# Performance work log

Hardware: AMD Instinct MI355X
Metric: run time of the kernel (lower is better)

## Reference

```python
import jax, jax.numpy as jnp
import numpy as np

E, T, D, H = 32, 65536, 512, 1024


def setup_inputs() -> dict:
    key = jax.random.key(0)
    k = jax.random.split(key, 7)
    norm = lambda kk, shp, sc: (jax.random.normal(kk, shp, jnp.float32) * sc)
    x = norm(k[0], (T, D), 1.0)
    w1 = norm(k[1], (E, D, H), D ** -0.5)   # per-expert up-proj (gate branch)
    b1 = norm(k[2], (E, H), 0.02)
    w3 = norm(k[3], (E, D, H), D ** -0.5)   # per-expert up-proj (linear branch)
    b3 = norm(k[4], (E, H), 0.02)
    w2 = norm(k[5], (E, H, D), H ** -0.5)   # per-expert down-proj
    b2 = norm(k[6], (E, D), 0.02)
    # tokens are pre-sorted by expert; uniform dispatch of T//E tokens per expert
    group_sizes = jnp.full((E,), T // E, jnp.int32)
    return dict(x=x, w1=w1, b1=b1, w3=w3, b3=b3, w2=w2, b2=b2,
                group_sizes=group_sizes)


def reference(x, w1, b1, w3, b3, w2, b2, group_sizes):
    # expert id per token, derived from contiguous group sizes
    bounds = jnp.cumsum(group_sizes)                       # [E]
    seg = jnp.searchsorted(bounds, jnp.arange(x.shape[0]), side='right')  # [T]
    # grouped GEMMs: per-expert weight bank applied to its contiguous token slab
    h1 = jax.lax.ragged_dot(x, w1, group_sizes) + b1[seg]  # [T,H]
    h3 = jax.lax.ragged_dot(x, w3, group_sizes) + b3[seg]  # [T,H]
    h = jax.nn.silu(h1) * h3                               # SwiGLU gate
    out = jax.lax.ragged_dot(h, w2, group_sizes) + b2[seg] # [T,D]
    return out
```

## Files before the change

kernel.cpp:

```cpp
#include <hip/hip_runtime.h>
#include <hip/hip_bf16.h>

#define TOK 65536
#define NE  32
#define DD  512
#define HH  1024
#define TPE 2048

typedef short s16x8  __attribute__((ext_vector_type(8)));
typedef float f32x16 __attribute__((ext_vector_type(16)));
using u16 = unsigned short;
using u32 = unsigned int;

__device__ __forceinline__ u16 f2bf(float f) {
  __bf16 h = (__bf16)f;
  return __builtin_bit_cast(u16, h);
}
__device__ __forceinline__ u32 pk2(float lo, float hi) {
  return (u32)f2bf(lo) | ((u32)f2bf(hi) << 16);
}
__device__ __forceinline__ int swz(int row, int colb) {
  return (row << 7) + (colb ^ ((row & 7) << 4));
}

#define MFMA(a, b, c) __builtin_amdgcn_mfma_f32_32x32x16_bf16(a, b, c, 0, 0, 0)
#define GLD(src, dst) __builtin_amdgcn_global_load_lds( \
    (const __attribute__((address_space(1))) void*)(src), \
    (__attribute__((address_space(3))) void*)(dst), 16, 0, 0)


__global__ __launch_bounds__(256) void p1_cvt_x(
    const float* __restrict__ x, u16* __restrict__ xb) {
  const size_t i = ((size_t)blockIdx.x * 256 + threadIdx.x) * 8;
  const float4 a = *(const float4*)(x + i);
  const float4 b = *(const float4*)(x + i + 4);
  uint4 v;
  v.x = pk2(a.x, a.y); v.y = pk2(a.z, a.w);
  v.z = pk2(b.x, b.y); v.w = pk2(b.z, b.w);
  *(uint4*)(xb + i) = v;
}

__global__ __launch_bounds__(256) void p2_w13t(
    const float* __restrict__ w1, const float* __restrict__ w3,
    u16* __restrict__ w13t) {
  __shared__ __align__(16) u16 L1[64 * 72], L3[64 * 72];
  const int bid = blockIdx.x;
  const int e = bid >> 7, rr = bid & 127;
  const int d0 = (rr & 7) << 6, h0 = (rr >> 3) << 6;
  const int t = threadIdx.x;
  const float* const s1 = w1 + (size_t)e * DD * HH + (size_t)d0 * HH + h0;
  const float* const s3 = w3 + (size_t)e * DD * HH + (size_t)d0 * HH + h0;
  const int cg = (t & 15) << 2, rbase = t >> 4;
#pragma unroll
  for (int j = 0; j < 4; ++j) {
    const int dr = rbase + (j << 4);
    const float4 a = *(const float4*)(s1 + (size_t)dr * HH + cg);
    const float4 b = *(const float4*)(s3 + (size_t)dr * HH + cg);
    L1[(cg + 0) * 72 + dr] = f2bf(a.x); L1[(cg + 1) * 72 + dr] = f2bf(a.y);
    L1[(cg + 2) * 72 + dr] = f2bf(a.z); L1[(cg + 3) * 72 + dr] = f2bf(a.w);
    L3[(cg + 0) * 72 + dr] = f2bf(b.x); L3[(cg + 1) * 72 + dr] = f2bf(b.y);
    L3[(cg + 2) * 72 + dr] = f2bf(b.z); L3[(cg + 3) * 72 + dr] = f2bf(b.w);
  }
  __syncthreads();
  u16* const dst = w13t + (size_t)e * (2 * HH) * DD;
  const int cb8 = (t & 7) << 3;
#pragma unroll
  for (int j = 0; j < 2; ++j) {
    const int nloc = (t >> 3) + (j << 5);
    const int n = h0 + nloc;
    const int R1 = ((n >> 5) << 6) + (n & 31);
    const uint4 v1 = *(const uint4*)(L1 + nloc * 72 + cb8);
    const uint4 v3 = *(const uint4*)(L3 + nloc * 72 + cb8);
    *(uint4*)(dst + (size_t)R1 * DD + d0 + cb8) = v1;
    *(uint4*)(dst + (size_t)(R1 + 32) * DD + d0 + cb8) = v3;
  }
}

__global__ __launch_bounds__(256) void p3_w2t(
    const float* __restrict__ w2, u16* __restrict__ w2t) {
  __shared__ __align__(16) u16 L[64 * 72];
  const int bid = blockIdx.x;
  const int e = bid >> 7, rr = bid & 127;
  const int d0 = (rr & 7) << 6, h0 = (rr >> 3) << 6;
  const int t = threadIdx.x;
  const float* const s = w2 + (size_t)e * HH * DD + (size_t)h0 * DD + d0;
  const int cg = (t & 15) << 2, rbase = t >> 4;
#pragma unroll
  for (int j = 0; j < 4; ++j) {
    const int hr = rbase + (j << 4);
    const float4 a = *(const float4*)(s + (size_t)hr * DD + cg);
    L[(cg + 0) * 72 + hr] = f2bf(a.x); L[(cg + 1) * 72 + hr] = f2bf(a.y);
    L[(cg + 2) * 72 + hr] = f2bf(a.z); L[(cg + 3) * 72 + hr] = f2bf(a.w);
  }
  __syncthreads();
  u16* const dst = w2t + (size_t)e * DD * HH;
  const int cb8 = (t & 7) << 3;
#pragma unroll
  for (int j = 0; j < 2; ++j) {
    const int dloc = (t >> 3) + (j << 5);
    const uint4 v = *(const uint4*)(L + dloc * 72 + cb8);
    *(uint4*)(dst + (size_t)(d0 + dloc) * HH + h0 + cb8) = v;
  }
}

template <int MODE>
__global__ __launch_bounds__(256, 3) void gemm_tile(
    const u16* __restrict__ A, const u16* __restrict__ Bm,
    const float* __restrict__ bx, const float* __restrict__ by,
    void* __restrict__ outp) {
  constexpr int K = MODE ? HH : DD;
  constexpr int NT = K >> 6;
  constexpr int NBLK = MODE ? 4 : 16;
  __shared__ __align__(16) char lds[32768];
  char* const As = lds;
  char* const Bs = lds + 16384;

  const int bid = blockIdx.x;
  const int e   = bid / (16 * NBLK);
  const int rr  = bid % (16 * NBLK);
  const int m_t = rr & 15;
  const int n_t = rr >> 4;
  const int rowbase = e * TPE + (m_t << 7);

  const int t = threadIdx.x, wv = t >> 6, lane = t & 63;
  const int l31 = lane & 31, half = lane >> 5;
  const int wm = wv >> 1, wn = wv & 1;

  const u16* const Abase = A + (size_t)rowbase * K;
  const u16* const Bbase = Bm + (size_t)e * NBLK * 128 * K + (size_t)n_t * 128 * K;

  int soff[4], lb[4];
#pragma unroll
  for (int j = 0; j < 4; ++j) {
    const int idx = (j << 8) + t;
    const int r = idx >> 3;
    const int cb = ((idx & 7) << 4) ^ ((r & 7) << 4);
    soff[j] = r * K + (cb >> 1);
    lb[j] = ((j << 8) + (wv << 6)) << 4;
  }

  f32x16 c00 = {}, c01 = {}, c10 = {}, c11 = {};
  const int sw  = (l31 & 7) << 4;
  const int ra0 = ((wm << 6) + l31) << 7, ra1 = ra0 + (32 << 7);
  const int rb0 = ((wn << 6) + l31) << 7, rb1 = rb0 + (32 << 7);

  for (int kt = 0; kt < NT; ++kt) {
    const u16* const Ak = Abase + (kt << 6);
    const u16* const Bk = Bbase + (kt << 6);
#pragma unroll
    for (int j = 0; j < 4; ++j) {
      GLD(Ak + soff[j], As + lb[j]);
      GLD(Bk + soff[j], Bs + lb[j]);
    }
    __syncthreads();
#pragma unroll
    for (int ks = 0; ks < 4; ++ks) {
      const int ko = ((ks << 5) + (half << 4)) ^ sw;
      const s16x8 a0 = *(const s16x8*)(As + ra0 + ko);
      const s16x8 a1 = *(const s16x8*)(As + ra1 + ko);
      const s16x8 b0 = *(const s16x8*)(Bs + rb0 + ko);
      const s16x8 b1 = *(const s16x8*)(Bs + rb1 + ko);
      c00 = MFMA(a0, b0, c00); c01 = MFMA(a0, b1, c01);
      c10 = MFMA(a1, b0, c10); c11 = MFMA(a1, b1, c11);
    }
    __syncthreads();
  }

  if constexpr (MODE == 0) {
    const int gcol = (n_t << 6) + (wn << 5) + l31;
    const float bv1 = bx[e * HH + gcol];
    const float bv3 = by[e * HH + gcol];
    u16* const hp = (u16*)outp;
#pragma unroll
    for (int mf = 0; mf < 2; ++mf) {
      const f32x16 A1 = mf ? c10 : c00;
      const f32x16 A3 = mf ? c11 : c01;
#pragma unroll
      for (int rg = 0; rg < 16; ++rg) {
        const int grow = rowbase + (wm << 6) + (mf << 5) +
                         (rg & 3) + ((rg >> 2) << 3) + (half << 2);
        const float s1 = A1[rg] + bv1;
        const float s3 = A3[rg] + bv3;
        hp[(size_t)grow * HH + gcol] = f2bf(s1 * s3 / (1.0f + __expf(-s1)));
      }
    }
  } else {
    float* const op = (float*)outp;
#pragma unroll
    for (int mf = 0; mf < 2; ++mf) {
#pragma unroll
      for (int fn = 0; fn < 2; ++fn) {
        const f32x16 C = mf ? (fn ? c11 : c10) : (fn ? c01 : c00);
        const int gcol = (n_t << 7) + (wn << 6) + (fn << 5) + l31;
        const float bv = bx[e * DD + gcol];
#pragma unroll
        for (int rg = 0; rg < 16; ++rg) {
          const int grow = rowbase + (wm << 6) + (mf << 5) +
                           (rg & 3) + ((rg >> 2) << 3) + (half << 2);
          op[(size_t)grow * DD + gcol] = C[rg] + bv;
        }
      }
    }
  }
}

__global__ __launch_bounds__(256, 2) void k1_up_swiglu(
    const float* __restrict__ x,  const float* __restrict__ w1,
    const float* __restrict__ b1, const float* __restrict__ w3,
    const float* __restrict__ b3, u16* __restrict__ hbuf) {
  __shared__ __align__(16) char lds[32768];
  char* const As  = lds;
  char* const B1s = lds + 16384;
  char* const B3s = lds + 24576;
  const int bid = blockIdx.x;
  const int e = bid >> 8, rr = bid & 255;
  const int m_t = rr & 15, n_t = rr >> 4;
  const int rowbase = e * TPE + (m_t << 7), colbase = n_t << 6;
  const int t = threadIdx.x, wv = t >> 6, lane = t & 63;
  const int l31 = lane & 31, half = lane >> 5;
  const int wm = wv >> 1, wn = wv & 1;
  const int ag = t & 15, am0 = t >> 4, bn = t & 63, bk0 = t >> 6;
  const float* const xb = x + (size_t)rowbase * DD + (ag << 2);
  const size_t woff = (size_t)e * (DD * HH) + colbase + bn;
  const float* const w1b = w1 + woff;
  const float* const w3b = w3 + woff;
  float4 ra[8]; float rb1[16], rb3[16];
  auto gload = [&](int kt) {
    const float* xp = xb + (kt << 6);
#pragma unroll
    for (int j = 0; j < 8; ++j)
      ra[j] = *(const float4*)(xp + (size_t)(am0 + (j << 4)) * DD);
#pragma unroll
    for (int j = 0; j < 2; ++j) {
      const int k0 = (kt << 6) + ((bk0 + (j << 2)) << 3);
#pragma unroll
      for (int i = 0; i < 8; ++i) {
        rb1[(j << 3) + i] = w1b[(size_t)(k0 + i) * HH];
        rb3[(j << 3) + i] = w3b[(size_t)(k0 + i) * HH];
      }
    }
  };
  f32x16 acc10 = {}, acc11 = {}, acc30 = {}, acc31 = {};
  gload(0);
  for (int kt = 0; kt < 8; ++kt) {
    if (kt) __syncthreads();
#pragma unroll
    for (int j = 0; j < 8; ++j) {
      const int m = am0 + (j << 4);
      uint2 v; v.x = pk2(ra[j].x, ra[j].y); v.y = pk2(ra[j].z, ra[j].w);
      *(uint2*)(As + swz(m, ag << 3)) = v;
    }
#pragma unroll
    for (int j = 0; j < 2; ++j) {
      const int kg = bk0 + (j << 2);
      uint4 v;
      v.x = pk2(rb1[(j << 3) + 0], rb1[(j << 3) + 1]);
      v.y = pk2(rb1[(j << 3) + 2], rb1[(j << 3) + 3]);
      v.z = pk2(rb1[(j << 3) + 4], rb1[(j << 3) + 5]);
      v.w = pk2(rb1[(j << 3) + 6], rb1[(j << 3) + 7]);
      *(uint4*)(B1s + swz(bn, kg << 4)) = v;
      v.x = pk2(rb3[(j << 3) + 0], rb3[(j << 3) + 1]);
      v.y = pk2(rb3[(j << 3) + 2], rb3[(j << 3) + 3]);
      v.z = pk2(rb3[(j << 3) + 4], rb3[(j << 3) + 5]);
      v.w = pk2(rb3[(j << 3) + 6], rb3[(j << 3) + 7]);
      *(uint4*)(B3s + swz(bn, kg << 4)) = v;
    }
    __syncthreads();
    if (kt < 7) gload(kt + 1);
#pragma unroll
    for (int kk = 0; kk < 4; ++kk) {
      const int colb = (kk << 5) + (half << 4);
      const s16x8 a0 = *(const s16x8*)(As  + swz((wm << 6) + l31,      colb));
      const s16x8 a1 = *(const s16x8*)(As  + swz((wm << 6) + 32 + l31, colb));
      const s16x8 f1 = *(const s16x8*)(B1s + swz((wn << 5) + l31,      colb));
      const s16x8 f3 = *(const s16x8*)(B3s + swz((wn << 5) + l31,      colb));
      acc10 = MFMA(a0, f1, acc10); acc30 = MFMA(a0, f3, acc30);
      acc11 = MFMA(a1, f1, acc11); acc31 = MFMA(a1, f3, acc31);
    }
  }
  const int gcol = colbase + (wn << 5) + l31;
  const float bv1 = b1[e * HH + gcol], bv3 = b3[e * HH + gcol];
  u16* const hp = hbuf + gcol;
#pragma unroll
  for (int mb = 0; mb < 2; ++mb) {
    const f32x16 A1 = mb ? acc11 : acc10;
    const f32x16 A3 = mb ? acc31 : acc30;
#pragma unroll
    for (int rg = 0; rg < 16; ++rg) {
      const int grow = rowbase + (wm << 6) + (mb << 5) +
                       (rg & 3) + ((rg >> 2) << 3) + (half << 2);
      const float s1 = A1[rg] + bv1, s3 = A3[rg] + bv3;
      hp[(size_t)grow * HH] = f2bf(s1 * s3 / (1.0f + __expf(-s1)));
    }
  }
}

__global__ __launch_bounds__(256, 2) void k2_down(
    const u16* __restrict__ hbuf, const float* __restrict__ w2,
    const float* __restrict__ b2, float* __restrict__ out) {
  __shared__ __align__(16) char lds[32768];
  char* const As = lds;
  char* const Bs = lds + 16384;
  const int bid = blockIdx.x;
  const int e = bid >> 6, rr = bid & 63;
  const int m_t = rr & 15, n_t = rr >> 4;
  const int rowbase = e * TPE + (m_t << 7), colbase = n_t << 7;
  const int t = threadIdx.x, wv = t >> 6, lane = t & 63;
  const int l31 = lane & 31, half = lane >> 5;
  const int wm = wv >> 1, wn = wv & 1;
  const int ag = t & 7, am0 = t >> 3, bnn = t & 127, bk0 = t >> 7;
  const u16* const hb = hbuf + (size_t)rowbase * HH + (ag << 3);
  const float* const w2b = w2 + (size_t)e * (HH * DD) + colbase + bnn;
  uint4 ra[4]; float rb[32];
  auto gload = [&](int kt) {
#pragma unroll
    for (int j = 0; j < 4; ++j)
      ra[j] = *(const uint4*)(hb + (size_t)(am0 + (j << 5)) * HH + (kt << 6));
#pragma unroll
    for (int j = 0; j < 4; ++j) {
      const int k0 = (kt << 6) + ((bk0 + (j << 1)) << 3);
#pragma unroll
      for (int i = 0; i < 8; ++i)
        rb[(j << 3) + i] = w2b[(size_t)(k0 + i) * DD];
    }
  };
  f32x16 c00 = {}, c01 = {}, c10 = {}, c11 = {};
  gload(0);
  for (int kt = 0; kt < 16; ++kt) {
    if (kt) __syncthreads();
#pragma unroll
    for (int j = 0; j < 4; ++j)
      *(uint4*)(As + swz(am0 + (j << 5), ag << 4)) = ra[j];
#pragma unroll
    for (int j = 0; j < 4; ++j) {
      const int kg = bk0 + (j << 1);
      uint4 v;
      v.x = pk2(rb[(j << 3) + 0], rb[(j << 3) + 1]);
      v.y = pk2(rb[(j << 3) + 2], rb[(j << 3) + 3]);
      v.z = pk2(rb[(j << 3) + 4], rb[(j << 3) + 5]);
      v.w = pk2(rb[(j << 3) + 6], rb[(j << 3) + 7]);
      *(uint4*)(Bs + swz(bnn, kg << 4)) = v;
    }
    __syncthreads();
    if (kt < 15) gload(kt + 1);
#pragma unroll
    for (int kk = 0; kk < 4; ++kk) {
      const int colb = (kk << 5) + (half << 4);
      const s16x8 af0 = *(const s16x8*)(As + swz((wm << 6) + l31,      colb));
      const s16x8 af1 = *(const s16x8*)(As + swz((wm << 6) + 32 + l31, colb));
      const s16x8 bf0 = *(const s16x8*)(Bs + swz((wn << 6) + l31,      colb));
      const s16x8 bf1 = *(const s16x8*)(Bs + swz((wn << 6) + 32 + l31, colb));
      c00 = MFMA(af0, bf0, c00); c01 = MFMA(af0, bf1, c01);
      c10 = MFMA(af1, bf0, c10); c11 = MFMA(af1, bf1, c11);
    }
  }
#pragma unroll
  for (int mb = 0; mb < 2; ++mb) {
#pragma unroll
    for (int nb = 0; nb < 2; ++nb) {
      const f32x16 c = mb ? (nb ? c11 : c10) : (nb ? c01 : c00);
      const int gcol = colbase + (wn << 6) + (nb << 5) + l31;
      const float bv = b2[e * DD + gcol];
#pragma unroll
      for (int rg = 0; rg < 16; ++rg) {
        const int grow = rowbase + (wm << 6) + (mb << 5) +
                         (rg & 3) + ((rg >> 2) << 3) + (half << 2);
        out[(size_t)grow * DD + gcol] = c[rg] + bv;
      }
    }
  }
}

extern "C" void kernel_launch(void* const* d_in, const int* in_sizes, int n_in,
                              void* d_out, int out_size, void* d_ws, size_t ws_size,
                              hipStream_t stream) {
  const float* x  = (const float*)d_in[0];
  const float* w1 = (const float*)d_in[1];
  const float* b1 = (const float*)d_in[2];
  const float* w3 = (const float*)d_in[3];
  const float* b3 = (const float*)d_in[4];
  const float* w2 = (const float*)d_in[5];
  const float* b2 = (const float*)d_in[6];

  const size_t W13T_B = (size_t)NE * 2 * HH * DD * 2;
  const size_t W2T_B  = (size_t)NE * DD * HH * 2;
  const size_t H_B    = (size_t)TOK * HH * 2;

  if (ws_size >= W13T_B + W2T_B + H_B) {
    u16* const xb   = (u16*)d_out;
    u16* const w13t = (u16*)d_ws;
    u16* const w2t  = (u16*)((char*)d_ws + W13T_B);
    u16* const hbuf = (u16*)((char*)d_ws + W13T_B + W2T_B);

    p1_cvt_x<<<dim3(TOK * DD / 2048), dim3(256), 0, stream>>>(x, xb);
    p2_w13t <<<dim3(NE * 128),        dim3(256), 0, stream>>>(w1, w3, w13t);
    p3_w2t  <<<dim3(NE * 128),        dim3(256), 0, stream>>>(w2, w2t);
    gemm_tile<0><<<dim3(NE * 256), dim3(256), 0, stream>>>(xb, w13t, b1, b3, hbuf);
    gemm_tile<1><<<dim3(NE * 64),  dim3(256), 0, stream>>>(hbuf, w2t, b2, nullptr, d_out);
  } else {
    u16* hbuf = (ws_size >= H_B) ? (u16*)d_ws : (u16*)d_out;
    k1_up_swiglu<<<dim3(NE * 256), dim3(256), 0, stream>>>(x, w1, b1, w3, b3, hbuf);
    k2_down<<<dim3(NE * 64), dim3(256), 0, stream>>>(hbuf, w2, b2, (float*)d_out);
  }
}
```

Before: 368.1 us.

## Use 256x256 tiles with 8 waves and double-buffered LDS in grouped GEMMs

Replaces the 128x128, 4-wave GEMM tile with a 256x256 tile computed by 512 threads. Each wave now holds a 128x64 accumulator block. Global-to-LDS loads are double-buffered across 128KB of LDS, with explicit vmcnt waits so the next K-slice is fetched during the current slice's MFMAs. MFMA bursts are wrapped in s_setprio. The goal is more operand reuse per LDS byte and hiding load latency, at the cost of far fewer blocks (2048 and 512) and higher register and LDS pressure, which limits occupancy.

```diff
diff --git a/kernel.cpp b/kernel.cpp
--- a/kernel.cpp
+++ b/kernel.cpp
@@ -27,7 +27,7 @@
 #define GLD(src, dst) __builtin_amdgcn_global_load_lds( \
     (const __attribute__((address_space(1))) void*)(src), \
     (__attribute__((address_space(3))) void*)(dst), 16, 0, 0)
-
+#define SETP(n) __builtin_amdgcn_s_setprio(n)
 
 __global__ __launch_bounds__(256) void p1_cvt_x(
     const float* __restrict__ x, u16* __restrict__ xb) {
@@ -104,100 +104,140 @@
 }
 
 template <int MODE>
-__global__ __launch_bounds__(256, 3) void gemm_tile(
+__global__ __launch_bounds__(512, 2) void gemm256(
     const u16* __restrict__ A, const u16* __restrict__ Bm,
     const float* __restrict__ bx, const float* __restrict__ by,
     void* __restrict__ outp) {
-  constexpr int K = MODE ? HH : DD;
+  constexpr int K  = MODE ? HH : DD;
   constexpr int NT = K >> 6;
-  constexpr int NBLK = MODE ? 4 : 16;
-  __shared__ __align__(16) char lds[32768];
-  char* const As = lds;
-  char* const Bs = lds + 16384;
+  constexpr int NB = MODE ? 2 : 8;
+  __shared__ __align__(16) char lds[131072];
 
   const int bid = blockIdx.x;
-  const int e   = bid / (16 * NBLK);
-  const int rr  = bid % (16 * NBLK);
-  const int m_t = rr & 15;
-  const int n_t = rr >> 4;
-  const int rowbase = e * TPE + (m_t << 7);
-
-  const int t = threadIdx.x, wv = t >> 6, lane = t & 63;
+  const int e   = bid / (8 * NB);
+  const int rr  = bid % (8 * NB);
+  const int m_t = rr & 7;
+  const int n_t = rr >> 3;
+  const int rowbase = e * TPE + (m_t << 8);
+
+  const int t = threadIdx.x;
+  const int wv = t >> 6, lane = t & 63;
   const int l31 = lane & 31, half = lane >> 5;
-  const int wm = wv >> 1, wn = wv & 1;
+  const int wm = wv >> 2, wn = wv & 3;
 
   const u16* const Abase = A + (size_t)rowbase * K;
-  const u16* const Bbase = Bm + (size_t)e * NBLK * 128 * K + (size_t)n_t * 128 * K;
-
-  int soff[4], lb[4];
+  const u16* const Bbase = Bm + ((size_t)e * NB + n_t) * 256 * K;
+
+  int soff[4];
 #pragma unroll
   for (int j = 0; j < 4; ++j) {
-    const int idx = (j << 8) + t;
-    const int r = idx >> 3;
-    const int cb = ((idx & 7) << 4) ^ ((r & 7) << 4);
-    soff[j] = r * K + (cb >> 1);
-    lb[j] = ((j << 8) + (wv << 6)) << 4;
-  }
-
-  f32x16 c00 = {}, c01 = {}, c10 = {}, c11 = {};
-  const int sw  = (l31 & 7) << 4;
-  const int ra0 = ((wm << 6) + l31) << 7, ra1 = ra0 + (32 << 7);
-  const int rb0 = ((wn << 6) + l31) << 7, rb1 = rb0 + (32 << 7);
-
-  for (int kt = 0; kt < NT; ++kt) {
+    const int c = (j << 9) + t;
+    const int r = c >> 3, ci = c & 7;
+    soff[j] = r * K + ((((ci << 4) ^ ((r & 7) << 4))) >> 1);
+  }
+  const int lbw = wv << 10;
+
+  auto stage = [&](int kt, int buf) {
+    char* const dA = lds + (buf << 16);
+    char* const dB = dA + 32768;
     const u16* const Ak = Abase + (kt << 6);
     const u16* const Bk = Bbase + (kt << 6);
 #pragma unroll
     for (int j = 0; j < 4; ++j) {
-      GLD(Ak + soff[j], As + lb[j]);
-      GLD(Bk + soff[j], Bs + lb[j]);
-    }
-    __syncthreads();
-#pragma unroll
-    for (int ks = 0; ks < 4; ++ks) {
-      const int ko = ((ks << 5) + (half << 4)) ^ sw;
-      const s16x8 a0 = *(const s16x8*)(As + ra0 + ko);
-      const s16x8 a1 = *(const s16x8*)(As + ra1 + ko);
-      const s16x8 b0 = *(const s16x8*)(Bs + rb0 + ko);
-      const s16x8 b1 = *(const s16x8*)(Bs + rb1 + ko);
-      c00 = MFMA(a0, b0, c00); c01 = MFMA(a0, b1, c01);
-      c10 = MFMA(a1, b0, c10); c11 = MFMA(a1, b1, c11);
-    }
-    __syncthreads();
-  }
+      GLD(Ak + soff[j], dA + (j << 13) + lbw);
+      GLD(Bk + soff[j], dB + (j << 13) + lbw);
+    }
+  };
+
+  const int swr = (l31 & 7) << 4;
+  f32x16 acc[4][2] = {};
+  s16x8 bb[2][2];
+
+#define LDA(As, mf, ks) \
+  (*(const s16x8*)((As) + (((wm << 7) + ((mf) << 5) + l31) << 7) + \
+                   ((((ks) << 5) + (half << 4)) ^ swr)))
+#define LDB(Bs, nf, ks) \
+  (*(const s16x8*)((Bs) + (((wn << 6) + ((nf) << 5) + l31) << 7) + \
+                   ((((ks) << 5) + (half << 4)) ^ swr)))
+#define PH_B(Bs, kh) \
+  bb[0][0] = LDB(Bs, 0, 2*(kh));     bb[0][1] = LDB(Bs, 1, 2*(kh)); \
+  bb[1][0] = LDB(Bs, 0, 2*(kh)+1);   bb[1][1] = LDB(Bs, 1, 2*(kh)+1);
+#define PH_AM(As, mh, kh) { \
+  const s16x8 x0 = LDA(As, 2*(mh),   2*(kh)); \
+  const s16x8 x1 = LDA(As, 2*(mh),   2*(kh)+1); \
+  const s16x8 x2 = LDA(As, 2*(mh)+1, 2*(kh)); \
+  const s16x8 x3 = LDA(As, 2*(mh)+1, 2*(kh)+1); \
+  SETP(1); \
+  acc[2*(mh)][0]   = MFMA(x0, bb[0][0], acc[2*(mh)][0]); \
+  acc[2*(mh)][1]   = MFMA(x0, bb[0][1], acc[2*(mh)][1]); \
+  acc[2*(mh)][0]   = MFMA(x1, bb[1][0], acc[2*(mh)][0]); \
+  acc[2*(mh)][1]   = MFMA(x1, bb[1][1], acc[2*(mh)][1]); \
+  acc[2*(mh)+1][0] = MFMA(x2, bb[0][0], acc[2*(mh)+1][0]); \
+  acc[2*(mh)+1][1] = MFMA(x2, bb[0][1], acc[2*(mh)+1][1]); \
+  acc[2*(mh)+1][0] = MFMA(x3, bb[1][0], acc[2*(mh)+1][0]); \
+  acc[2*(mh)+1][1] = MFMA(x3, bb[1][1], acc[2*(mh)+1][1]); \
+  SETP(0); }
+
+  stage(0, 0);
+  for (int kt = 0; kt < NT; ++kt) {
+    const int cur = kt & 1;
+    if (kt + 1 < NT) {
+      stage(kt + 1, cur ^ 1);
+      asm volatile("s_waitcnt vmcnt(8)" ::: "memory");
+    } else {
+      asm volatile("s_waitcnt vmcnt(0)" ::: "memory");
+    }
+    __builtin_amdgcn_s_barrier();
+    __builtin_amdgcn_sched_barrier(0);
+    {
+      const char* const As = lds + (cur << 16);
+      const char* const Bs = As + 32768;
+      PH_B(Bs, 0);
+      PH_AM(As, 0, 0);
+      PH_AM(As, 1, 0);
+      PH_B(Bs, 1);
+      PH_AM(As, 0, 1);
+      PH_AM(As, 1, 1);
+    }
+    asm volatile("s_waitcnt lgkmcnt(0)" ::: "memory");
+    __builtin_amdgcn_sched_barrier(0);
+    __builtin_amdgcn_s_barrier();
+  }
+#undef LDA
+#undef LDB
+#undef PH_B
+#undef PH_AM
 
   if constexpr (MODE == 0) {
-    const int gcol = (n_t << 6) + (wn << 5) + l31;
-    const float bv1 = bx[e * HH + gcol];
-    const float bv3 = by[e * HH + gcol];
+    const int g = (n_t << 2) + wn;
+    const int hcol = (g << 5) + l31;
+    const float bv1 = bx[e * HH + hcol];
+    const float bv3 = by[e * HH + hcol];
     u16* const hp = (u16*)outp;
 #pragma unroll
-    for (int mf = 0; mf < 2; ++mf) {
-      const f32x16 A1 = mf ? c10 : c00;
-      const f32x16 A3 = mf ? c11 : c01;
+    for (int mf = 0; mf < 4; ++mf) {
 #pragma unroll
       for (int rg = 0; rg < 16; ++rg) {
-        const int grow = rowbase + (wm << 6) + (mf << 5) +
+        const int grow = rowbase + (wm << 7) + (mf << 5) +
                          (rg & 3) + ((rg >> 2) << 3) + (half << 2);
-        const float s1 = A1[rg] + bv1;
-        const float s3 = A3[rg] + bv3;
-        hp[(size_t)grow * HH + gcol] = f2bf(s1 * s3 / (1.0f + __expf(-s1)));
+        const float s1 = acc[mf][0][rg] + bv1;
+        const float s3 = acc[mf][1][rg] + bv3;
+        hp[(size_t)grow * HH + hcol] = f2bf(s1 * s3 / (1.0f + __expf(-s1)));
       }
     }
   } else {
     float* const op = (float*)outp;
 #pragma unroll
-    for (int mf = 0; mf < 2; ++mf) {
-#pragma unroll
-      for (int fn = 0; fn < 2; ++fn) {
-        const f32x16 C = mf ? (fn ? c11 : c10) : (fn ? c01 : c00);
-        const int gcol = (n_t << 7) + (wn << 6) + (fn << 5) + l31;
-        const float bv = bx[e * DD + gcol];
+    for (int mf = 0; mf < 4; ++mf) {
+#pragma unroll
+      for (int nf = 0; nf < 2; ++nf) {
+        const int col = (n_t << 8) + (wn << 6) + (nf << 5) + l31;
+        const float bv = bx[e * DD + col];
 #pragma unroll
         for (int rg = 0; rg < 16; ++rg) {
-          const int grow = rowbase + (wm << 6) + (mf << 5) +
+          const int grow = rowbase + (wm << 7) + (mf << 5) +
                            (rg & 3) + ((rg >> 2) << 3) + (half << 2);
-          op[(size_t)grow * DD + gcol] = C[rg] + bv;
+          op[(size_t)grow * DD + col] = acc[mf][nf][rg] + bv;
         }
       }
     }
@@ -395,8 +435,8 @@
     p1_cvt_x<<<dim3(TOK * DD / 2048), dim3(256), 0, stream>>>(x, xb);
     p2_w13t <<<dim3(NE * 128),        dim3(256), 0, stream>>>(w1, w3, w13t);
     p3_w2t  <<<dim3(NE * 128),        dim3(256), 0, stream>>>(w2, w2t);
-    gemm_tile<0><<<dim3(NE * 256), dim3(256), 0, stream>>>(xb, w13t, b1, b3, hbuf);
-    gemm_tile<1><<<dim3(NE * 64),  dim3(256), 0, stream>>>(hbuf, w2t, b2, nullptr, d_out);
+    gemm256<0><<<dim3(NE * 64), dim3(512), 0, stream>>>(xb, w13t, b1, b3, hbuf);
+    gemm256<1><<<dim3(NE * 16), dim3(512), 0, stream>>>(hbuf, w2t, b2, nullptr, d_out);
   } else {
     u16* hbuf = (ws_size >= H_B) ? (u16*)d_ws : (u16*)d_out;
     k1_up_swiglu<<<dim3(NE * 256), dim3(256), 0, stream>>>(x, w1, b1, w3, b3, hbuf);
```

Result: slower. 386.5 us (+5.0%).

## Fuse x fp32-to-bf16 conversion into up-GEMM, merge weight prep kernels, swizzle blocks

Applied to the files above, without the earlier changes.

Drops the separate x conversion kernel. The up-projection GEMM now loads fp32 x into registers, converts it to bf16 and writes it into swizzled LDS, prefetching the next K tile while the MFMAs run. The two weight-transpose kernels are merged into one launch, and both GEMMs remap block IDs in groups of 8 and raise the occupancy hint to 4. This removes a full write and re-read of the bf16 copy of x plus two launches, at the cost of more registers and VALU conversion work inside the GEMM loop.

```diff
diff --git a/kernel.cpp b/kernel.cpp
--- a/kernel.cpp
+++ b/kernel.cpp
@@ -28,96 +28,78 @@
     (const __attribute__((address_space(1))) void*)(src), \
     (__attribute__((address_space(3))) void*)(dst), 16, 0, 0)
 
-
-__global__ __launch_bounds__(256) void p1_cvt_x(
-    const float* __restrict__ x, u16* __restrict__ xb) {
-  const size_t i = ((size_t)blockIdx.x * 256 + threadIdx.x) * 8;
-  const float4 a = *(const float4*)(x + i);
-  const float4 b = *(const float4*)(x + i + 4);
-  uint4 v;
-  v.x = pk2(a.x, a.y); v.y = pk2(a.z, a.w);
-  v.z = pk2(b.x, b.y); v.w = pk2(b.z, b.w);
-  *(uint4*)(xb + i) = v;
-}
-
-__global__ __launch_bounds__(256) void p2_w13t(
+__global__ __launch_bounds__(256) void p23_wt(
     const float* __restrict__ w1, const float* __restrict__ w3,
-    u16* __restrict__ w13t) {
+    const float* __restrict__ w2,
+    u16* __restrict__ w13t, u16* __restrict__ w2t) {
   __shared__ __align__(16) u16 L1[64 * 72], L3[64 * 72];
-  const int bid = blockIdx.x;
-  const int e = bid >> 7, rr = bid & 127;
-  const int d0 = (rr & 7) << 6, h0 = (rr >> 3) << 6;
+  const int bid0 = blockIdx.x;
   const int t = threadIdx.x;
-  const float* const s1 = w1 + (size_t)e * DD * HH + (size_t)d0 * HH + h0;
-  const float* const s3 = w3 + (size_t)e * DD * HH + (size_t)d0 * HH + h0;
   const int cg = (t & 15) << 2, rbase = t >> 4;
-#pragma unroll
-  for (int j = 0; j < 4; ++j) {
-    const int dr = rbase + (j << 4);
-    const float4 a = *(const float4*)(s1 + (size_t)dr * HH + cg);
-    const float4 b = *(const float4*)(s3 + (size_t)dr * HH + cg);
-    L1[(cg + 0) * 72 + dr] = f2bf(a.x); L1[(cg + 1) * 72 + dr] = f2bf(a.y);
-    L1[(cg + 2) * 72 + dr] = f2bf(a.z); L1[(cg + 3) * 72 + dr] = f2bf(a.w);
-    L3[(cg + 0) * 72 + dr] = f2bf(b.x); L3[(cg + 1) * 72 + dr] = f2bf(b.y);
-    L3[(cg + 2) * 72 + dr] = f2bf(b.z); L3[(cg + 3) * 72 + dr] = f2bf(b.w);
-  }
-  __syncthreads();
-  u16* const dst = w13t + (size_t)e * (2 * HH) * DD;
   const int cb8 = (t & 7) << 3;
-#pragma unroll
-  for (int j = 0; j < 2; ++j) {
-    const int nloc = (t >> 3) + (j << 5);
-    const int n = h0 + nloc;
-    const int R1 = ((n >> 5) << 6) + (n & 31);
-    const uint4 v1 = *(const uint4*)(L1 + nloc * 72 + cb8);
-    const uint4 v3 = *(const uint4*)(L3 + nloc * 72 + cb8);
-    *(uint4*)(dst + (size_t)R1 * DD + d0 + cb8) = v1;
-    *(uint4*)(dst + (size_t)(R1 + 32) * DD + d0 + cb8) = v3;
-  }
-}
-
-__global__ __launch_bounds__(256) void p3_w2t(
-    const float* __restrict__ w2, u16* __restrict__ w2t) {
-  __shared__ __align__(16) u16 L[64 * 72];
-  const int bid = blockIdx.x;
-  const int e = bid >> 7, rr = bid & 127;
-  const int d0 = (rr & 7) << 6, h0 = (rr >> 3) << 6;
-  const int t = threadIdx.x;
-  const float* const s = w2 + (size_t)e * HH * DD + (size_t)h0 * DD + d0;
-  const int cg = (t & 15) << 2, rbase = t >> 4;
-#pragma unroll
-  for (int j = 0; j < 4; ++j) {
-    const int hr = rbase + (j << 4);
-    const float4 a = *(const float4*)(s + (size_t)hr * DD + cg);
-    L[(cg + 0) * 72 + hr] = f2bf(a.x); L[(cg + 1) * 72 + hr] = f2bf(a.y);
-    L[(cg + 2) * 72 + hr] = f2bf(a.z); L[(cg + 3) * 72 + hr] = f2bf(a.w);
-  }
-  __syncthreads();
-  u16* const dst = w2t + (size_t)e * DD * HH;
-  const int cb8 = (t & 7) << 3;
-#pragma unroll
-  for (int j = 0; j < 2; ++j) {
-    const int dloc = (t >> 3) + (j << 5);
-    const uint4 v = *(const uint4*)(L + dloc * 72 + cb8);
-    *(uint4*)(dst + (size_t)(d0 + dloc) * HH + h0 + cb8) = v;
-  }
-}
-
-template <int MODE>
-__global__ __launch_bounds__(256, 3) void gemm_tile(
-    const u16* __restrict__ A, const u16* __restrict__ Bm,
-    const float* __restrict__ bx, const float* __restrict__ by,
-    void* __restrict__ outp) {
-  constexpr int K = MODE ? HH : DD;
-  constexpr int NT = K >> 6;
-  constexpr int NBLK = MODE ? 4 : 16;
+
+  if (bid0 < NE * 128) {
+    const int e = bid0 >> 7, rr = bid0 & 127;
+    const int d0 = (rr & 7) << 6, h0 = (rr >> 3) << 6;
+    const float* const s1 = w1 + (size_t)e * DD * HH + (size_t)d0 * HH + h0;
+    const float* const s3 = w3 + (size_t)e * DD * HH + (size_t)d0 * HH + h0;
+#pragma unroll
+    for (int j = 0; j < 4; ++j) {
+      const int dr = rbase + (j << 4);
+      const float4 a = *(const float4*)(s1 + (size_t)dr * HH + cg);
+      const float4 b = *(const float4*)(s3 + (size_t)dr * HH + cg);
+      L1[(cg + 0) * 72 + dr] = f2bf(a.x); L1[(cg + 1) * 72 + dr] = f2bf(a.y);
+      L1[(cg + 2) * 72 + dr] = f2bf(a.z); L1[(cg + 3) * 72 + dr] = f2bf(a.w);
+      L3[(cg + 0) * 72 + dr] = f2bf(b.x); L3[(cg + 1) * 72 + dr] = f2bf(b.y);
+      L3[(cg + 2) * 72 + dr] = f2bf(b.z); L3[(cg + 3) * 72 + dr] = f2bf(b.w);
+    }
+    __syncthreads();
+    u16* const dst = w13t + (size_t)e * (2 * HH) * DD;
+#pragma unroll
+    for (int j = 0; j < 2; ++j) {
+      const int nloc = (t >> 3) + (j << 5);
+      const int n = h0 + nloc;
+      const int R1 = ((n >> 5) << 6) + (n & 31);
+      const uint4 v1 = *(const uint4*)(L1 + nloc * 72 + cb8);
+      const uint4 v3 = *(const uint4*)(L3 + nloc * 72 + cb8);
+      *(uint4*)(dst + (size_t)R1 * DD + d0 + cb8) = v1;
+      *(uint4*)(dst + (size_t)(R1 + 32) * DD + d0 + cb8) = v3;
+    }
+  } else {
+    const int bid = bid0 - NE * 128;
+    const int e = bid >> 7, rr = bid & 127;
+    const int d0 = (rr & 7) << 6, h0 = (rr >> 3) << 6;
+    const float* const s = w2 + (size_t)e * HH * DD + (size_t)h0 * DD + d0;
+#pragma unroll
+    for (int j = 0; j < 4; ++j) {
+      const int hr = rbase + (j << 4);
+      const float4 a = *(const float4*)(s + (size_t)hr * DD + cg);
+      L1[(cg + 0) * 72 + hr] = f2bf(a.x); L1[(cg + 1) * 72 + hr] = f2bf(a.y);
+      L1[(cg + 2) * 72 + hr] = f2bf(a.z); L1[(cg + 3) * 72 + hr] = f2bf(a.w);
+    }
+    __syncthreads();
+    u16* const dst = w2t + (size_t)e * DD * HH;
+#pragma unroll
+    for (int j = 0; j < 2; ++j) {
+      const int dloc = (t >> 3) + (j << 5);
+      const uint4 v = *(const uint4*)(L1 + dloc * 72 + cb8);
+      *(uint4*)(dst + (size_t)(d0 + dloc) * HH + h0 + cb8) = v;
+    }
+  }
+}
+
+__global__ __launch_bounds__(256, 4) void g0_up(
+    const float* __restrict__ x, const u16* __restrict__ w13t,
+    const float* __restrict__ b1, const float* __restrict__ b3,
+    u16* __restrict__ hbuf) {
   __shared__ __align__(16) char lds[32768];
   char* const As = lds;
   char* const Bs = lds + 16384;
 
-  const int bid = blockIdx.x;
-  const int e   = bid / (16 * NBLK);
-  const int rr  = bid % (16 * NBLK);
+  int bid = blockIdx.x;
+  bid = (bid & 7) * (NE * 256 / 8) + (bid >> 3);
+  const int e   = bid >> 8;
+  const int rr  = bid & 255;
   const int m_t = rr & 15;
   const int n_t = rr >> 4;
   const int rowbase = e * TPE + (m_t << 7);
@@ -126,16 +108,25 @@
   const int l31 = lane & 31, half = lane >> 5;
   const int wm = wv >> 1, wn = wv & 1;
 
-  const u16* const Abase = A + (size_t)rowbase * K;
-  const u16* const Bbase = Bm + (size_t)e * NBLK * 128 * K + (size_t)n_t * 128 * K;
-
+  const int ag  = t & 15;
+  const int am0 = t >> 4;
+  const float* const xb = x + (size_t)rowbase * DD + (ag << 2);
+  float4 ra[8];
+  auto loadA = [&](int kt) {
+    const float* xp = xb + (kt << 6);
+#pragma unroll
+    for (int j = 0; j < 8; ++j)
+      ra[j] = *(const float4*)(xp + (size_t)(am0 + (j << 4)) * DD);
+  };
+
+  const u16* const Bbase = w13t + ((size_t)e * 2048 + (size_t)n_t * 128) * DD;
   int soff[4], lb[4];
 #pragma unroll
   for (int j = 0; j < 4; ++j) {
     const int idx = (j << 8) + t;
     const int r = idx >> 3;
     const int cb = ((idx & 7) << 4) ^ ((r & 7) << 4);
-    soff[j] = r * K + (cb >> 1);
+    soff[j] = r * DD + (cb >> 1);
     lb[j] = ((j << 8) + (wv << 6)) << 4;
   }
 
@@ -144,15 +135,20 @@
   const int ra0 = ((wm << 6) + l31) << 7, ra1 = ra0 + (32 << 7);
   const int rb0 = ((wn << 6) + l31) << 7, rb1 = rb0 + (32 << 7);
 
-  for (int kt = 0; kt < NT; ++kt) {
-    const u16* const Ak = Abase + (kt << 6);
+  loadA(0);
+  for (int kt = 0; kt < 8; ++kt) {
+    if (kt) __syncthreads();
+#pragma unroll
+    for (int j = 0; j < 8; ++j) {
+      const int m = am0 + (j << 4);
+      uint2 v; v.x = pk2(ra[j].x, ra[j].y); v.y = pk2(ra[j].z, ra[j].w);
+      *(uint2*)(As + swz(m, ag << 3)) = v;
+    }
     const u16* const Bk = Bbase + (kt << 6);
 #pragma unroll
-    for (int j = 0; j < 4; ++j) {
-      GLD(Ak + soff[j], As + lb[j]);
-      GLD(Bk + soff[j], Bs + lb[j]);
-    }
-    __syncthreads();
+    for (int j = 0; j < 4; ++j) GLD(Bk + soff[j], Bs + lb[j]);
+    __syncthreads();
+    if (kt < 7) loadA(kt + 1);
 #pragma unroll
     for (int ks = 0; ks < 4; ++ks) {
       const int ko = ((ks << 5) + (half << 4)) ^ sw;
@@ -163,42 +159,97 @@
       c00 = MFMA(a0, b0, c00); c01 = MFMA(a0, b1, c01);
       c10 = MFMA(a1, b0, c10); c11 = MFMA(a1, b1, c11);
     }
-    __syncthreads();
-  }
-
-  if constexpr (MODE == 0) {
-    const int gcol = (n_t << 6) + (wn << 5) + l31;
-    const float bv1 = bx[e * HH + gcol];
-    const float bv3 = by[e * HH + gcol];
-    u16* const hp = (u16*)outp;
-#pragma unroll
-    for (int mf = 0; mf < 2; ++mf) {
-      const f32x16 A1 = mf ? c10 : c00;
-      const f32x16 A3 = mf ? c11 : c01;
+  }
+
+  const int hcol = (n_t << 6) + (wn << 5) + l31;
+  const float bv1 = b1[e * HH + hcol];
+  const float bv3 = b3[e * HH + hcol];
+#pragma unroll
+  for (int mf = 0; mf < 2; ++mf) {
+    const f32x16 A1 = mf ? c10 : c00;
+    const f32x16 A3 = mf ? c11 : c01;
+#pragma unroll
+    for (int rg = 0; rg < 16; ++rg) {
+      const int grow = rowbase + (wm << 6) + (mf << 5) +
+                       (rg & 3) + ((rg >> 2) << 3) + (half << 2);
+      const float s1 = A1[rg] + bv1;
+      const float s3 = A3[rg] + bv3;
+      hbuf[(size_t)grow * HH + hcol] = f2bf(s1 * s3 / (1.0f + __expf(-s1)));
+    }
+  }
+}
+
+__global__ __launch_bounds__(256, 4) void g1_down(
+    const u16* __restrict__ hbuf, const u16* __restrict__ w2t,
+    const float* __restrict__ b2, float* __restrict__ out) {
+  __shared__ __align__(16) char lds[32768];
+  char* const As = lds;
+  char* const Bs = lds + 16384;
+
+  int bid = blockIdx.x;
+  bid = (bid & 7) * (NE * 64 / 8) + (bid >> 3);
+  const int e   = bid >> 6;
+  const int rr  = bid & 63;
+  const int m_t = rr & 15;
+  const int n_t = rr >> 4;
+  const int rowbase = e * TPE + (m_t << 7);
+
+  const int t = threadIdx.x, wv = t >> 6, lane = t & 63;
+  const int l31 = lane & 31, half = lane >> 5;
+  const int wm = wv >> 1, wn = wv & 1;
+
+  const u16* const Abase = hbuf + (size_t)rowbase * HH;
+  const u16* const Bbase = w2t + ((size_t)e * DD + (size_t)n_t * 128) * HH;
+
+  int soff[4], lb[4];
+#pragma unroll
+  for (int j = 0; j < 4; ++j) {
+    const int idx = (j << 8) + t;
+    const int r = idx >> 3;
+    const int cb = ((idx & 7) << 4) ^ ((r & 7) << 4);
+    soff[j] = r * HH + (cb >> 1);
+    lb[j] = ((j << 8) + (wv << 6)) << 4;
+  }
+
+  f32x16 c00 = {}, c01 = {}, c10 = {}, c11 = {};
+  const int sw  = (l31 & 7) << 4;
+  const int ra0 = ((wm << 6) + l31) << 7, ra1 = ra0 + (32 << 7);
+  const int rb0 = ((wn << 6) + l31) << 7, rb1 = rb0 + (32 << 7);
+
+  for (int kt = 0; kt < 16; ++kt) {
+    const u16* const Ak = Abase + (kt << 6);
+    const u16* const Bk = Bbase + (kt << 6);
+#pragma unroll
+    for (int j = 0; j < 4; ++j) {
+      GLD(Ak + soff[j], As + lb[j]);
+      GLD(Bk + soff[j], Bs + lb[j]);
+    }
+    __syncthreads();
+#pragma unroll
+    for (int ks = 0; ks < 4; ++ks) {
+      const int ko = ((ks << 5) + (half << 4)) ^ sw;
+      const s16x8 a0 = *(const s16x8*)(As + ra0 + ko);
+      const s16x8 a1 = *(const s16x8*)(As + ra1 + ko);
+      const s16x8 b0 = *(const s16x8*)(Bs + rb0 + ko);
+      const s16x8 b1 = *(const s16x8*)(Bs + rb1 + ko);
+      c00 = MFMA(a0, b0, c00); c01 = MFMA(a0, b1, c01);
+      c10 = MFMA(a1, b0, c10); c11 = MFMA(a1, b1, c11);
+    }
+    __syncthreads();
+  }
+
+#pragma unroll
+  for (int mf = 0; mf < 2; ++mf) {
+#pragma unroll
+    for (int nf = 0; nf < 2; ++nf) {
+      const f32x16 c = mf ? (nf ? c11 : c10) : (nf ? c01 : c00);
+      const int gcol = (n_t << 7) + (wn << 6) + (nf << 5) + l31;
+      const float bv = b2[e * DD + gcol];
 #pragma unroll
       for (int rg = 0; rg < 16; ++rg) {
         const int grow = rowbase + (wm << 6) + (mf << 5) +
                          (rg & 3) + ((rg >> 2) << 3) + (half << 2);
-        const float s1 = A1[rg] + bv1;
-        const float s3 = A3[rg] + bv3;
-        hp[(size_t)grow * HH + gcol] = f2bf(s1 * s3 / (1.0f + __expf(-s1)));
-      }
-    }
-  } else {
-    float* const op = (float*)outp;
-#pragma unroll
-    for (int mf = 0; mf < 2; ++mf) {
-#pragma unroll
-      for (int fn = 0; fn < 2; ++fn) {
-        const f32x16 C = mf ? (fn ? c11 : c10) : (fn ? c01 : c00);
-        const int gcol = (n_t << 7) + (wn << 6) + (fn << 5) + l31;
-        const float bv = bx[e * DD + gcol];
-#pragma unroll
-        for (int rg = 0; rg < 16; ++rg) {
-          const int grow = rowbase + (wm << 6) + (mf << 5) +
-                           (rg & 3) + ((rg >> 2) << 3) + (half << 2);
-          op[(size_t)grow * DD + gcol] = C[rg] + bv;
-        }
+        out[(size_t)grow * DD + gcol] = c[rg] + bv;
       }
     }
   }
@@ -387,16 +438,13 @@
   const size_t H_B    = (size_t)TOK * HH * 2;
 
   if (ws_size >= W13T_B + W2T_B + H_B) {
-    u16* const xb   = (u16*)d_out;
     u16* const w13t = (u16*)d_ws;
     u16* const w2t  = (u16*)((char*)d_ws + W13T_B);
     u16* const hbuf = (u16*)((char*)d_ws + W13T_B + W2T_B);
 
-    p1_cvt_x<<<dim3(TOK * DD / 2048), dim3(256), 0, stream>>>(x, xb);
-    p2_w13t <<<dim3(NE * 128),        dim3(256), 0, stream>>>(w1, w3, w13t);
-    p3_w2t  <<<dim3(NE * 128),        dim3(256), 0, stream>>>(w2, w2t);
-    gemm_tile<0><<<dim3(NE * 256), dim3(256), 0, stream>>>(xb, w13t, b1, b3, hbuf);
-    gemm_tile<1><<<dim3(NE * 64),  dim3(256), 0, stream>>>(hbuf, w2t, b2, nullptr, d_out);
+    p23_wt <<<dim3(NE * 256), dim3(256), 0, stream>>>(w1, w3, w2, w13t, w2t);
+    g0_up  <<<dim3(NE * 256), dim3(256), 0, stream>>>(x, w13t, b1, b3, hbuf);
+    g1_down<<<dim3(NE * 64),  dim3(256), 0, stream>>>(hbuf, w2t, b2, (float*)d_out);
   } else {
     u16* hbuf = (ws_size >= H_B) ? (u16*)d_ws : (u16*)d_out;
     k1_up_swiglu<<<dim3(NE * 256), dim3(256), 0, stream>>>(x, w1, b1, w3, b3, hbuf);
```

New measurement: 528.0 us. 1.43x slower.
